# Performance work log

Hardware: AMD Instinct MI355X
Metric: run time of the kernel (lower is better)

The kernel has to match this reference:

```python
import jax, jax.numpy as jnp
import numpy as np
import math

B, T, D, H = 4, 2048, 1024, 16
HD = D // H  # 64

def setup_inputs() -> dict:
    key = jax.random.key(0)
    ks = jax.random.split(key, 11)
    s = 1.0 / math.sqrt(D)
    return {
        "q": jax.random.normal(ks[0], (B, T, D), jnp.float32),
        "k": jax.random.normal(ks[1], (B, T, D), jnp.float32),
        "v": jax.random.normal(ks[2], (B, T, D), jnp.float32),
        "Wq": jax.random.normal(ks[3], (D, D), jnp.float32) * s,
        "bq": jnp.zeros((D,), jnp.float32),
        "Wk": jax.random.normal(ks[4], (D, D), jnp.float32) * s,
        "bk": jnp.zeros((D,), jnp.float32),
        "Wv": jax.random.normal(ks[5], (D, D), jnp.float32) * s,
        "bv": jnp.zeros((D,), jnp.float32),
        "Wo": jax.random.normal(ks[6], (D, D), jnp.float32) * s,
        "bo": jnp.zeros((D,), jnp.float32),
    }

def reference(q, k, v, Wq, bq, Wk, bk, Wv, bv, Wo, bo):
    # Linear projections (torch Linear: x @ W.T + b)
    qp = q @ Wq.T + bq
    kp = k @ Wk.T + bk
    vp = v @ Wv.T + bv
    # [B, T, D] -> [B, H, T, HD]
    def split(x):
        return x.reshape(B, T, H, HD).transpose(0, 2, 1, 3)
    qh, kh, vh = split(qp), split(kp), split(vp)
    # scaled dot-product attention
    score = jnp.einsum('bhqd,bhkd->bhqk', qh, kh) / math.sqrt(HD)
    attn = jax.nn.softmax(score, axis=-1)
    out = jnp.einsum('bhqk,bhkd->bhqd', attn, vh)
    # merge heads and output projection
    out = out.transpose(0, 2, 1, 3).reshape(B, T, D)
    return out @ Wo.T + bo
```

## Files before the change

kernel.cpp:

```cpp
#include <hip/hip_runtime.h>
#include <hip/hip_bf16.h>
#include <stdint.h>

#define B_ 4
#define T_ 2048
#define D_ 1024
#define H_ 16
#define HD_ 64
#define NKT (T_ / 64)

typedef __bf16 bf16;
typedef __bf16 bf16x8 __attribute__((ext_vector_type(8)));
typedef __bf16 bf16x4 __attribute__((ext_vector_type(4)));
typedef float f32x4 __attribute__((ext_vector_type(4)));
typedef uint32_t u32x4 __attribute__((ext_vector_type(4)));

#define QSCALE 0.18033688011112042f

__device__ __forceinline__ float fast_exp2(float x) {
#if __has_builtin(__builtin_amdgcn_exp2f)
    return __builtin_amdgcn_exp2f(x);
#else
    return exp2f(x);
#endif
}

__device__ __forceinline__ void async_load16(const bf16* g, const bf16* lds_uniform) {
    __builtin_amdgcn_global_load_lds(
        (const __attribute__((address_space(1))) uint32_t*)(uintptr_t)g,
        (__attribute__((address_space(3))) uint32_t*)(uintptr_t)lds_uniform,
        16, 0, 0);
}

__device__ __forceinline__ uint32_t pack2_bf16(float lo, float hi) {
    union { uint32_t u; __bf16 h[2]; } r;
    r.h[0] = (__bf16)lo;
    r.h[1] = (__bf16)hi;
    return r.u;
}

__device__ __forceinline__ void permswap16(uint32_t& a, uint32_t& b) {
    asm("v_permlane16_swap_b32 %0, %1" : "+v"(a), "+v"(b));
}

__global__ __launch_bounds__(256) void cast3(const float* __restrict__ s0, bf16* __restrict__ d0,
                                             const float* __restrict__ s1, bf16* __restrict__ d1,
                                             const float* __restrict__ s2, bf16* __restrict__ d2,
                                             int n4) {
    const float* s = blockIdx.y == 0 ? s0 : (blockIdx.y == 1 ? s1 : s2);
    bf16* d = blockIdx.y == 0 ? d0 : (blockIdx.y == 1 ? d1 : d2);
    int i = blockIdx.x * 256 + threadIdx.x;
    if (i < n4) {
        f32x4 v = ((const f32x4*)s)[i];
        bf16x4 o;
        o.x = (bf16)v.x; o.y = (bf16)v.y; o.z = (bf16)v.z; o.w = (bf16)v.w;
        ((bf16x4*)d)[i] = o;
    }
}

__global__ __launch_bounds__(256) void cast4(const float* __restrict__ s0, bf16* __restrict__ d0,
                                             const float* __restrict__ s1, bf16* __restrict__ d1,
                                             const float* __restrict__ s2, bf16* __restrict__ d2,
                                             const float* __restrict__ s3, bf16* __restrict__ d3,
                                             int n4) {
    const float* s = blockIdx.y == 0 ? s0 : (blockIdx.y == 1 ? s1 : (blockIdx.y == 2 ? s2 : s3));
    bf16* d = blockIdx.y == 0 ? d0 : (blockIdx.y == 1 ? d1 : (blockIdx.y == 2 ? d2 : d3));
    int i = blockIdx.x * 256 + threadIdx.x;
    if (i < n4) {
        f32x4 v = ((const f32x4*)s)[i];
        bf16x4 o;
        o.x = (bf16)v.x; o.y = (bf16)v.y; o.z = (bf16)v.z; o.w = (bf16)v.w;
        ((bf16x4*)d)[i] = o;
    }
}

template <typename OutT, int VMODE>
__global__ __launch_bounds__(256) void gemm_nt(const bf16* __restrict__ A,
                                               const bf16* __restrict__ W,
                                               const float* __restrict__ bias,
                                               OutT* __restrict__ C,
                                               int M, int N, int K, float scale) {
    __shared__ bf16 As[2][128 * 32];
    __shared__ bf16 Bs[2][128 * 32];
    const int tid = threadIdx.x;
    const int wid = tid >> 6, lane = tid & 63;
    const int quad = lane >> 4, l15 = lane & 15;
    const int wm = (wid >> 1) * 64, wn = (wid & 1) * 64;
    const int bx = N >> 7;
    const int lin = blockIdx.x;
    const int ty = (lin & 7) + 8 * (lin / (8 * bx));
    const int tx = (lin >> 3) % bx;
    const long rowA0 = (long)ty * 128;
    const long rowB0 = (long)tx * 128;
    const int srow = lane >> 2;
    const int schunk = (lane & 3) * 8;
    const int sbase = (wid * 32) * 32;

    f32x4 acc[4][4];
#pragma unroll
    for (int i = 0; i < 4; i++)
#pragma unroll
        for (int j = 0; j < 4; j++) acc[i][j] = (f32x4){0.f, 0.f, 0.f, 0.f};

#pragma unroll
    for (int s = 0; s < 2; s++) {
        int r = wid * 32 + s * 16 + srow;
        async_load16(&A[(rowA0 + r) * K + schunk], &As[0][sbase + s * 16 * 32]);
        async_load16(&W[(rowB0 + r) * K + schunk], &Bs[0][sbase + s * 16 * 32]);
    }
    __syncthreads();

    const int NIT = K >> 5;
    for (int it = 0; it < NIT; it++) {
        const int cur = it & 1;
        if (it + 1 < NIT) {
            const int k1 = (it + 1) << 5, nb = cur ^ 1;
#pragma unroll
            for (int s = 0; s < 2; s++) {
                int r = wid * 32 + s * 16 + srow;
                async_load16(&A[(rowA0 + r) * K + k1 + schunk], &As[nb][sbase + s * 16 * 32]);
                async_load16(&W[(rowB0 + r) * K + k1 + schunk], &Bs[nb][sbase + s * 16 * 32]);
            }
        }
        bf16x8 af[4], bfr[4];
#pragma unroll
        for (int i = 0; i < 4; i++)
            af[i] = *(const bf16x8*)&As[cur][(wm + i * 16 + l15) * 32 + quad * 8];
#pragma unroll
        for (int j = 0; j < 4; j++)
            bfr[j] = *(const bf16x8*)&Bs[cur][(wn + j * 16 + l15) * 32 + quad * 8];
#pragma unroll
        for (int i = 0; i < 4; i++)
#pragma unroll
            for (int j = 0; j < 4; j++)
                acc[i][j] = __builtin_amdgcn_mfma_f32_16x16x32_bf16(af[i], bfr[j],
                                                                    acc[i][j], 0, 0, 0);
        __syncthreads();
    }

    if constexpr (VMODE == 0) {
#pragma unroll
        for (int i = 0; i < 4; i++) {
            long m = rowA0 + wm + i * 16 + quad * 4;
#pragma unroll
            for (int j = 0; j < 4; j++) {
                long n = rowB0 + wn + j * 16 + l15;
                float bb = bias[n];
#pragma unroll
                for (int r = 0; r < 4; r++) {
                    float v = (acc[i][j][r] + bb) * scale;
                    C[(m + r) * N + n] = (OutT)v;
                }
            }
        }
    } else {
        __shared__ bf16 Tt[128 * 136];
#pragma unroll
        for (int i = 0; i < 4; i++) {
            int ml = wm + i * 16 + quad * 4;
#pragma unroll
            for (int j = 0; j < 4; j++) {
                int nl = wn + j * 16 + l15;
                float bb = bias[rowB0 + nl];
                bf16x4 ov = {(bf16)(acc[i][j][0] + bb), (bf16)(acc[i][j][1] + bb),
                             (bf16)(acc[i][j][2] + bb), (bf16)(acc[i][j][3] + bb)};
                *(bf16x4*)&Tt[nl * 136 + ml] = ov;
            }
        }
        __syncthreads();
        const long bidx = rowA0 >> 11;
        const int t0 = (int)(rowA0 & 2047);
#pragma unroll
        for (int p = 0; p < 8; p++) {
            int nl = p * 16 + (tid >> 4);
            int c = tid & 15;
            bf16x8 val = *(const bf16x8*)&Tt[nl * 136 + c * 8];
            int n = (int)rowB0 + nl;
            long vrow = (bidx * H_ + (n >> 6)) * (long)HD_ + (n & 63);
            int cp = (c & ~3) | ((c & 1) << 1) | ((c & 2) >> 1);
            *(bf16x8*)&((bf16*)C)[vrow * T_ + t0 + cp * 8] = val;
        }
    }
}

__global__ __launch_bounds__(256) void attn_kernel(const bf16* __restrict__ Qp,
                                                   const bf16* __restrict__ Kp,
                                                   const bf16* __restrict__ VT,
                                                   bf16* __restrict__ Op) {
    __shared__ bf16 smem[4][64 * 64];
    const int tid = threadIdx.x;
    const int wid = tid >> 6, lane = tid & 63;
    const int quad = lane >> 4, l15 = lane & 15;
    const int q7 = l15 & 7;
    const int lin = blockIdx.x;
    const int bh = (lin & 7) + 8 * (lin >> 6);
    const int qt = (lin >> 3) & 7;
    const int b = bh >> 4, h = bh & 15;
    const long tok0 = (long)b * T_ + (long)qt * 256 + wid * 64;
    const int hcol = h * HD_;
    const long vrow0 = ((long)bh) * HD_;
    const int g_sw = ((lane & 7) ^ (lane >> 3)) * 8;
    const int srow = lane >> 3;
    const int sbase = (wid * 16) * 64;

    {
        const long krow0 = (long)b * T_;
#pragma unroll
        for (int s = 0; s < 2; s++) {
            int r = wid * 16 + s * 8 + srow;
            async_load16(&Kp[(krow0 + r) * D_ + hcol + g_sw], &smem[0][sbase + s * 8 * 64]);
            async_load16(&VT[(vrow0 + r) * T_ + g_sw], &smem[2][sbase + s * 8 * 64]);
        }
    }

    bf16x8 bq[4][2];
#pragma unroll
    for (int nt = 0; nt < 4; nt++)
#pragma unroll
        for (int ks = 0; ks < 2; ks++)
            bq[nt][ks] = *(const bf16x8*)&Qp[(tok0 + nt * 16 + l15) * D_ + hcol +
                                             ks * 32 + quad * 8];

    f32x4 o[4][4];
#pragma unroll
    for (int mt = 0; mt < 4; mt++)
#pragma unroll
        for (int nt = 0; nt < 4; nt++) o[mt][nt] = (f32x4){0.f, 0.f, 0.f, 0.f};
    float lsum[4] = {0.f, 0.f, 0.f, 0.f};

    __syncthreads();

    for (int kt = 0; kt < NKT; kt++) {
        const int cur = kt & 1;
        if (kt + 1 < NKT) {
            const long krow1 = (long)b * T_ + (long)(kt + 1) * 64;
            const int nb = cur ^ 1;
#pragma unroll
            for (int s = 0; s < 2; s++) {
                int r = wid * 16 + s * 8 + srow;
                async_load16(&Kp[(krow1 + r) * D_ + hcol + g_sw], &smem[nb][sbase + s * 8 * 64]);
                async_load16(&VT[(vrow0 + r) * T_ + (long)(kt + 1) * 64 + g_sw],
                             &smem[2 + nb][sbase + s * 8 * 64]);
            }
        }
        const bf16* Ksc = smem[cur];
        const bf16* Vsc = smem[2 + cur];

        bf16x8 pb0[4];
        {
            uint32_t pA[2][4], pB[2][4];
#pragma unroll
            for (int mt = 0; mt < 2; mt++) {
                bf16x8 ak0 = *(const bf16x8*)&Ksc[(mt * 16 + l15) * 64 + ((quad ^ q7) * 8)];
                bf16x8 ak1 = *(const bf16x8*)&Ksc[(mt * 16 + l15) * 64 + (((4 + quad) ^ q7) * 8)];
#pragma unroll
                for (int nt = 0; nt < 4; nt++) {
                    f32x4 s = {0.f, 0.f, 0.f, 0.f};
                    s = __builtin_amdgcn_mfma_f32_16x16x32_bf16(ak0, bq[nt][0], s, 0, 0, 0);
                    s = __builtin_amdgcn_mfma_f32_16x16x32_bf16(ak1, bq[nt][1], s, 0, 0, 0);
                    float p0 = fast_exp2(s[0]), p1 = fast_exp2(s[1]);
                    float p2 = fast_exp2(s[2]), p3 = fast_exp2(s[3]);
                    lsum[nt] += (p0 + p1) + (p2 + p3);
                    pA[mt][nt] = pack2_bf16(p0, p1);
                    pB[mt][nt] = pack2_bf16(p2, p3);
                }
            }
#pragma unroll
            for (int nt = 0; nt < 4; nt++) {
                permswap16(pA[0][nt], pA[1][nt]);
                permswap16(pB[0][nt], pB[1][nt]);
                u32x4 f = {pA[0][nt], pB[0][nt], pA[1][nt], pB[1][nt]};
                pb0[nt] = __builtin_bit_cast(bf16x8, f);
            }
        }
#pragma unroll
        for (int mt = 0; mt < 4; mt++) {
            bf16x8 av0 = *(const bf16x8*)&Vsc[(mt * 16 + l15) * 64 + ((quad ^ q7) * 8)];
#pragma unroll
            for (int nt = 0; nt < 4; nt++)
                o[mt][nt] = __builtin_amdgcn_mfma_f32_16x16x32_bf16(av0, pb0[nt],
                                                                    o[mt][nt], 0, 0, 0);
        }
        bf16x8 pb1[4];
        {
            uint32_t pA[2][4], pB[2][4];
#pragma unroll
            for (int mt = 0; mt < 2; mt++) {
                bf16x8 ak0 = *(const bf16x8*)&Ksc[((2 + mt) * 16 + l15) * 64 + ((quad ^ q7) * 8)];
                bf16x8 ak1 = *(const bf16x8*)&Ksc[((2 + mt) * 16 + l15) * 64 +
                                                  (((4 + quad) ^ q7) * 8)];
#pragma unroll
                for (int nt = 0; nt < 4; nt++) {
                    f32x4 s = {0.f, 0.f, 0.f, 0.f};
                    s = __builtin_amdgcn_mfma_f32_16x16x32_bf16(ak0, bq[nt][0], s, 0, 0, 0);
                    s = __builtin_amdgcn_mfma_f32_16x16x32_bf16(ak1, bq[nt][1], s, 0, 0, 0);
                    float p0 = fast_exp2(s[0]), p1 = fast_exp2(s[1]);
                    float p2 = fast_exp2(s[2]), p3 = fast_exp2(s[3]);
                    lsum[nt] += (p0 + p1) + (p2 + p3);
                    pA[mt][nt] = pack2_bf16(p0, p1);
                    pB[mt][nt] = pack2_bf16(p2, p3);
                }
            }
#pragma unroll
            for (int nt = 0; nt < 4; nt++) {
                permswap16(pA[0][nt], pA[1][nt]);
                permswap16(pB[0][nt], pB[1][nt]);
                u32x4 f = {pA[0][nt], pB[0][nt], pA[1][nt], pB[1][nt]};
                pb1[nt] = __builtin_bit_cast(bf16x8, f);
            }
        }
#pragma unroll
        for (int mt = 0; mt < 4; mt++) {
            bf16x8 av1 = *(const bf16x8*)&Vsc[(mt * 16 + l15) * 64 + (((4 + quad) ^ q7) * 8)];
#pragma unroll
            for (int nt = 0; nt < 4; nt++)
                o[mt][nt] = __builtin_amdgcn_mfma_f32_16x16x32_bf16(av1, pb1[nt],
                                                                    o[mt][nt], 0, 0, 0);
        }
        __syncthreads();
    }

#pragma unroll
    for (int nt = 0; nt < 4; nt++) {
        lsum[nt] += __shfl_xor(lsum[nt], 16, 64);
        lsum[nt] += __shfl_xor(lsum[nt], 32, 64);
        lsum[nt] = 1.f / lsum[nt];
    }

    bf16* ew = &smem[wid][0];
#pragma unroll
    for (int mt = 0; mt < 4; mt++)
#pragma unroll
        for (int nt = 0; nt < 4; nt++) {
            bf16x4 ov = {(bf16)(o[mt][nt][0] * lsum[nt]), (bf16)(o[mt][nt][1] * lsum[nt]),
                         (bf16)(o[mt][nt][2] * lsum[nt]), (bf16)(o[mt][nt][3] * lsum[nt])};
            *(bf16x4*)&ew[(nt * 16 + l15) * 64 +
                          (((mt * 2 + (quad >> 1)) ^ q7) * 8) + (quad & 1) * 4] = ov;
        }
#pragma unroll
    for (int p2 = 0; p2 < 8; p2++) {
        int q = p2 * 8 + (lane >> 3);
        int dc = lane & 7;
        bf16x8 ov = *(const bf16x8*)&ew[q * 64 + ((dc ^ (q & 7)) * 8)];
        *(bf16x8*)&Op[(tok0 + q) * D_ + hcol + dc * 8] = ov;
    }
}

extern "C" void kernel_launch(void* const* d_in, const int* in_sizes, int n_in,
                              void* d_out, int out_size, void* d_ws, size_t ws_size,
                              hipStream_t stream) {
    const float* q  = (const float*)d_in[0];
    const float* k  = (const float*)d_in[1];
    const float* v  = (const float*)d_in[2];
    const float* Wq = (const float*)d_in[3];
    const float* bq = (const float*)d_in[4];
    const float* Wk = (const float*)d_in[5];
    const float* bk = (const float*)d_in[6];
    const float* Wv = (const float*)d_in[7];
    const float* bv = (const float*)d_in[8];
    const float* Wo = (const float*)d_in[9];
    const float* bo = (const float*)d_in[10];
    float* out = (float*)d_out;

    const size_t MD = (size_t)B_ * T_ * D_;
    const size_t DD = (size_t)D_ * D_;
    char* ws = (char*)d_ws;
    bf16* Xq  = (bf16*)ws; ws += MD * 2;
    bf16* Xk  = (bf16*)ws; ws += MD * 2;
    bf16* Xv  = (bf16*)ws; ws += MD * 2;
    bf16* WqB = (bf16*)ws; ws += DD * 2;
    bf16* WkB = (bf16*)ws; ws += DD * 2;
    bf16* WvB = (bf16*)ws; ws += DD * 2;
    bf16* WoB = (bf16*)ws; ws += DD * 2;
    bf16* Qp  = (bf16*)ws; ws += MD * 2;
    bf16* Kp  = (bf16*)ws; ws += MD * 2;
    bf16* VtG = (bf16*)ws; ws += MD * 2;
    bf16* Op  = (bf16*)ws; ws += MD * 2;

    cast3<<<dim3(MD / 4 / 256, 3), 256, 0, stream>>>(q, Xq, k, Xk, v, Xv, MD / 4);
    cast4<<<dim3(DD / 4 / 256, 4), 256, 0, stream>>>(Wq, WqB, Wk, WkB, Wv, WvB, Wo, WoB, DD / 4);

    const int nblk = (B_ * T_ / 128) * (D_ / 128);
    gemm_nt<bf16, 0><<<nblk, 256, 0, stream>>>(Xq, WqB, bq, Qp, B_ * T_, D_, D_, QSCALE);
    gemm_nt<bf16, 0><<<nblk, 256, 0, stream>>>(Xk, WkB, bk, Kp, B_ * T_, D_, D_, 1.f);
    gemm_nt<bf16, 1><<<nblk, 256, 0, stream>>>(Xv, WvB, bv, VtG, B_ * T_, D_, D_, 1.f);

    attn_kernel<<<B_ * H_ * (T_ / 256), 256, 0, stream>>>(Qp, Kp, VtG, Op);

    gemm_nt<float, 0><<<nblk, 256, 0, stream>>>(Op, WoB, bo, out, B_ * T_, D_, D_, 1.f);
}
```

Measured before the change: 342.8 us.

## Merge QKV GEMMs into one launch and halve attention query tile per block

The three projection GEMMs now run as a single 1536-block launch, with a branch on blockIdx choosing the Q, K or V path. Shared memory is overlaid so the V-transpose staging buffer reuses the A/B tile space. The attention kernel now handles 32 queries per wave (128 per block) instead of 64, which doubles the grid to 1024 blocks, and it adds a launch bound of 4 blocks per CU. The aim is to fill the GPU better and cut launch gaps and tail effects, at the cost of loading each K/V tile twice as often per query.

```diff
diff --git a/kernel.cpp b/kernel.cpp
--- a/kernel.cpp
+++ b/kernel.cpp
@@ -75,19 +75,18 @@
 }
 
 template <typename OutT, int VMODE>
-__global__ __launch_bounds__(256) void gemm_nt(const bf16* __restrict__ A,
-                                               const bf16* __restrict__ W,
-                                               const float* __restrict__ bias,
-                                               OutT* __restrict__ C,
-                                               int M, int N, int K, float scale) {
-    __shared__ bf16 As[2][128 * 32];
-    __shared__ bf16 Bs[2][128 * 32];
+__device__ __forceinline__ void gemm_body(const bf16* __restrict__ A,
+                                          const bf16* __restrict__ W,
+                                          const float* __restrict__ bias,
+                                          OutT* __restrict__ C,
+                                          int lin, float scale,
+                                          bf16* As, bf16* Bs, bf16* Tt) {
+    const int K = D_, N = D_;
     const int tid = threadIdx.x;
     const int wid = tid >> 6, lane = tid & 63;
     const int quad = lane >> 4, l15 = lane & 15;
     const int wm = (wid >> 1) * 64, wn = (wid & 1) * 64;
     const int bx = N >> 7;
-    const int lin = blockIdx.x;
     const int ty = (lin & 7) + 8 * (lin / (8 * bx));
     const int tx = (lin >> 3) % bx;
     const long rowA0 = (long)ty * 128;
@@ -105,30 +104,32 @@
 #pragma unroll
     for (int s = 0; s < 2; s++) {
         int r = wid * 32 + s * 16 + srow;
-        async_load16(&A[(rowA0 + r) * K + schunk], &As[0][sbase + s * 16 * 32]);
-        async_load16(&W[(rowB0 + r) * K + schunk], &Bs[0][sbase + s * 16 * 32]);
+        async_load16(&A[(rowA0 + r) * K + schunk], &As[sbase + s * 16 * 32]);
+        async_load16(&W[(rowB0 + r) * K + schunk], &Bs[sbase + s * 16 * 32]);
     }
     __syncthreads();
 
     const int NIT = K >> 5;
     for (int it = 0; it < NIT; it++) {
         const int cur = it & 1;
+        const int co = cur * (128 * 32);
         if (it + 1 < NIT) {
-            const int k1 = (it + 1) << 5, nb = cur ^ 1;
+            const int k1 = (it + 1) << 5;
+            const int no = (cur ^ 1) * (128 * 32);
 #pragma unroll
             for (int s = 0; s < 2; s++) {
                 int r = wid * 32 + s * 16 + srow;
-                async_load16(&A[(rowA0 + r) * K + k1 + schunk], &As[nb][sbase + s * 16 * 32]);
-                async_load16(&W[(rowB0 + r) * K + k1 + schunk], &Bs[nb][sbase + s * 16 * 32]);
+                async_load16(&A[(rowA0 + r) * K + k1 + schunk], &As[no + sbase + s * 16 * 32]);
+                async_load16(&W[(rowB0 + r) * K + k1 + schunk], &Bs[no + sbase + s * 16 * 32]);
             }
         }
         bf16x8 af[4], bfr[4];
 #pragma unroll
         for (int i = 0; i < 4; i++)
-            af[i] = *(const bf16x8*)&As[cur][(wm + i * 16 + l15) * 32 + quad * 8];
+            af[i] = *(const bf16x8*)&As[co + (wm + i * 16 + l15) * 32 + quad * 8];
 #pragma unroll
         for (int j = 0; j < 4; j++)
-            bfr[j] = *(const bf16x8*)&Bs[cur][(wn + j * 16 + l15) * 32 + quad * 8];
+            bfr[j] = *(const bf16x8*)&Bs[co + (wn + j * 16 + l15) * 32 + quad * 8];
 #pragma unroll
         for (int i = 0; i < 4; i++)
 #pragma unroll
@@ -154,7 +155,6 @@
             }
         }
     } else {
-        __shared__ bf16 Tt[128 * 136];
 #pragma unroll
         for (int i = 0; i < 4; i++) {
             int ml = wm + i * 16 + quad * 4;
@@ -183,20 +183,56 @@
     }
 }
 
-__global__ __launch_bounds__(256) void attn_kernel(const bf16* __restrict__ Qp,
-                                                   const bf16* __restrict__ Kp,
-                                                   const bf16* __restrict__ VT,
-                                                   bf16* __restrict__ Op) {
+__global__ __launch_bounds__(256) void gemm_qkv(const bf16* __restrict__ Xq,
+                                                const bf16* __restrict__ WqB,
+                                                const float* __restrict__ bq,
+                                                bf16* __restrict__ Qp,
+                                                const bf16* __restrict__ Xk,
+                                                const bf16* __restrict__ WkB,
+                                                const float* __restrict__ bk,
+                                                bf16* __restrict__ Kp,
+                                                const bf16* __restrict__ Xv,
+                                                const bf16* __restrict__ WvB,
+                                                const float* __restrict__ bv,
+                                                bf16* __restrict__ VtG) {
+    __shared__ __align__(16) char sm[34816];
+    bf16* As = (bf16*)sm;
+    bf16* Bs = (bf16*)(sm + 16384);
+    bf16* Tt = (bf16*)sm;
+    const int p = blockIdx.x >> 9;
+    const int lin = blockIdx.x & 511;
+    if (p == 0)
+        gemm_body<bf16, 0>(Xq, WqB, bq, Qp, lin, QSCALE, As, Bs, Tt);
+    else if (p == 1)
+        gemm_body<bf16, 0>(Xk, WkB, bk, Kp, lin, 1.f, As, Bs, Tt);
+    else
+        gemm_body<bf16, 1>(Xv, WvB, bv, VtG, lin, 1.f, As, Bs, Tt);
+}
+
+__global__ __launch_bounds__(256) void gemm_out(const bf16* __restrict__ Op,
+                                                const bf16* __restrict__ WoB,
+                                                const float* __restrict__ bo,
+                                                float* __restrict__ out) {
+    __shared__ __align__(16) char sm[32768];
+    bf16* As = (bf16*)sm;
+    bf16* Bs = (bf16*)(sm + 16384);
+    gemm_body<float, 0>(Op, WoB, bo, out, blockIdx.x, 1.f, As, Bs, nullptr);
+}
+
+__global__ __launch_bounds__(256, 4) void attn_kernel(const bf16* __restrict__ Qp,
+                                                      const bf16* __restrict__ Kp,
+                                                      const bf16* __restrict__ VT,
+                                                      bf16* __restrict__ Op) {
     __shared__ bf16 smem[4][64 * 64];
     const int tid = threadIdx.x;
     const int wid = tid >> 6, lane = tid & 63;
     const int quad = lane >> 4, l15 = lane & 15;
     const int q7 = l15 & 7;
     const int lin = blockIdx.x;
-    const int bh = (lin & 7) + 8 * (lin >> 6);
-    const int qt = (lin >> 3) & 7;
+    const int bh = (lin & 7) + 8 * (lin >> 7);
+    const int qt = (lin >> 3) & 15;
     const int b = bh >> 4, h = bh & 15;
-    const long tok0 = (long)b * T_ + (long)qt * 256 + wid * 64;
+    const long tok0 = (long)b * T_ + (long)qt * 128 + wid * 32;
     const int hcol = h * HD_;
     const long vrow0 = ((long)bh) * HD_;
     const int g_sw = ((lane & 7) ^ (lane >> 3)) * 8;
@@ -213,20 +249,20 @@
         }
     }
 
-    bf16x8 bq[4][2];
-#pragma unroll
-    for (int nt = 0; nt < 4; nt++)
+    bf16x8 bq[2][2];
+#pragma unroll
+    for (int nt = 0; nt < 2; nt++)
 #pragma unroll
         for (int ks = 0; ks < 2; ks++)
             bq[nt][ks] = *(const bf16x8*)&Qp[(tok0 + nt * 16 + l15) * D_ + hcol +
                                              ks * 32 + quad * 8];
 
-    f32x4 o[4][4];
+    f32x4 o[4][2];
 #pragma unroll
     for (int mt = 0; mt < 4; mt++)
 #pragma unroll
-        for (int nt = 0; nt < 4; nt++) o[mt][nt] = (f32x4){0.f, 0.f, 0.f, 0.f};
-    float lsum[4] = {0.f, 0.f, 0.f, 0.f};
+        for (int nt = 0; nt < 2; nt++) o[mt][nt] = (f32x4){0.f, 0.f, 0.f, 0.f};
+    float lsum[2] = {0.f, 0.f};
 
     __syncthreads();
 
@@ -246,15 +282,15 @@
         const bf16* Ksc = smem[cur];
         const bf16* Vsc = smem[2 + cur];
 
-        bf16x8 pb0[4];
+        bf16x8 pb0[2];
         {
-            uint32_t pA[2][4], pB[2][4];
+            uint32_t pA[2][2], pB[2][2];
 #pragma unroll
             for (int mt = 0; mt < 2; mt++) {
                 bf16x8 ak0 = *(const bf16x8*)&Ksc[(mt * 16 + l15) * 64 + ((quad ^ q7) * 8)];
                 bf16x8 ak1 = *(const bf16x8*)&Ksc[(mt * 16 + l15) * 64 + (((4 + quad) ^ q7) * 8)];
 #pragma unroll
-                for (int nt = 0; nt < 4; nt++) {
+                for (int nt = 0; nt < 2; nt++) {
                     f32x4 s = {0.f, 0.f, 0.f, 0.f};
                     s = __builtin_amdgcn_mfma_f32_16x16x32_bf16(ak0, bq[nt][0], s, 0, 0, 0);
                     s = __builtin_amdgcn_mfma_f32_16x16x32_bf16(ak1, bq[nt][1], s, 0, 0, 0);
@@ -266,7 +302,7 @@
                 }
             }
 #pragma unroll
-            for (int nt = 0; nt < 4; nt++) {
+            for (int nt = 0; nt < 2; nt++) {
                 permswap16(pA[0][nt], pA[1][nt]);
                 permswap16(pB[0][nt], pB[1][nt]);
                 u32x4 f = {pA[0][nt], pB[0][nt], pA[1][nt], pB[1][nt]};
@@ -277,20 +313,20 @@
         for (int mt = 0; mt < 4; mt++) {
             bf16x8 av0 = *(const bf16x8*)&Vsc[(mt * 16 + l15) * 64 + ((quad ^ q7) * 8)];
 #pragma unroll
-            for (int nt = 0; nt < 4; nt++)
+            for (int nt = 0; nt < 2; nt++)
                 o[mt][nt] = __builtin_amdgcn_mfma_f32_16x16x32_bf16(av0, pb0[nt],
                                                                     o[mt][nt], 0, 0, 0);
         }
-        bf16x8 pb1[4];
+        bf16x8 pb1[2];
         {
-            uint32_t pA[2][4], pB[2][4];
+            uint32_t pA[2][2], pB[2][2];
 #pragma unroll
             for (int mt = 0; mt < 2; mt++) {
                 bf16x8 ak0 = *(const bf16x8*)&Ksc[((2 + mt) * 16 + l15) * 64 + ((quad ^ q7) * 8)];
                 bf16x8 ak1 = *(const bf16x8*)&Ksc[((2 + mt) * 16 + l15) * 64 +
                                                   (((4 + quad) ^ q7) * 8)];
 #pragma unroll
-                for (int nt = 0; nt < 4; nt++) {
+                for (int nt = 0; nt < 2; nt++) {
                     f32x4 s = {0.f, 0.f, 0.f, 0.f};
                     s = __builtin_amdgcn_mfma_f32_16x16x32_bf16(ak0, bq[nt][0], s, 0, 0, 0);
                     s = __builtin_amdgcn_mfma_f32_16x16x32_bf16(ak1, bq[nt][1], s, 0, 0, 0);
@@ -302,7 +338,7 @@
                 }
             }
 #pragma unroll
-            for (int nt = 0; nt < 4; nt++) {
+            for (int nt = 0; nt < 2; nt++) {
                 permswap16(pA[0][nt], pA[1][nt]);
                 permswap16(pB[0][nt], pB[1][nt]);
                 u32x4 f = {pA[0][nt], pB[0][nt], pA[1][nt], pB[1][nt]};
@@ -313,7 +349,7 @@
         for (int mt = 0; mt < 4; mt++) {
             bf16x8 av1 = *(const bf16x8*)&Vsc[(mt * 16 + l15) * 64 + (((4 + quad) ^ q7) * 8)];
 #pragma unroll
-            for (int nt = 0; nt < 4; nt++)
+            for (int nt = 0; nt < 2; nt++)
                 o[mt][nt] = __builtin_amdgcn_mfma_f32_16x16x32_bf16(av1, pb1[nt],
                                                                     o[mt][nt], 0, 0, 0);
         }
@@ -321,7 +357,7 @@
     }
 
 #pragma unroll
-    for (int nt = 0; nt < 4; nt++) {
+    for (int nt = 0; nt < 2; nt++) {
         lsum[nt] += __shfl_xor(lsum[nt], 16, 64);
         lsum[nt] += __shfl_xor(lsum[nt], 32, 64);
         lsum[nt] = 1.f / lsum[nt];
@@ -331,14 +367,14 @@
 #pragma unroll
     for (int mt = 0; mt < 4; mt++)
 #pragma unroll
-        for (int nt = 0; nt < 4; nt++) {
+        for (int nt = 0; nt < 2; nt++) {
             bf16x4 ov = {(bf16)(o[mt][nt][0] * lsum[nt]), (bf16)(o[mt][nt][1] * lsum[nt]),
                          (bf16)(o[mt][nt][2] * lsum[nt]), (bf16)(o[mt][nt][3] * lsum[nt])};
             *(bf16x4*)&ew[(nt * 16 + l15) * 64 +
                           (((mt * 2 + (quad >> 1)) ^ q7) * 8) + (quad & 1) * 4] = ov;
         }
 #pragma unroll
-    for (int p2 = 0; p2 < 8; p2++) {
+    for (int p2 = 0; p2 < 4; p2++) {
         int q = p2 * 8 + (lane >> 3);
         int dc = lane & 7;
         bf16x8 ov = *(const bf16x8*)&ew[q * 64 + ((dc ^ (q & 7)) * 8)];
@@ -380,12 +416,9 @@
     cast3<<<dim3(MD / 4 / 256, 3), 256, 0, stream>>>(q, Xq, k, Xk, v, Xv, MD / 4);
     cast4<<<dim3(DD / 4 / 256, 4), 256, 0, stream>>>(Wq, WqB, Wk, WkB, Wv, WvB, Wo, WoB, DD / 4);
 
-    const int nblk = (B_ * T_ / 128) * (D_ / 128);
-    gemm_nt<bf16, 0><<<nblk, 256, 0, stream>>>(Xq, WqB, bq, Qp, B_ * T_, D_, D_, QSCALE);
-    gemm_nt<bf16, 0><<<nblk, 256, 0, stream>>>(Xk, WkB, bk, Kp, B_ * T_, D_, D_, 1.f);
-    gemm_nt<bf16, 1><<<nblk, 256, 0, stream>>>(Xv, WvB, bv, VtG, B_ * T_, D_, D_, 1.f);
-
-    attn_kernel<<<B_ * H_ * (T_ / 256), 256, 0, stream>>>(Qp, Kp, VtG, Op);
-
-    gemm_nt<float, 0><<<nblk, 256, 0, stream>>>(Op, WoB, bo, out, B_ * T_, D_, D_, 1.f);
-}
+    gemm_qkv<<<3 * 512, 256, 0, stream>>>(Xq, WqB, bq, Qp, Xk, WkB, bk, Kp, Xv, WvB, bv, VtG);
+
+    attn_kernel<<<B_ * H_ * (T_ / 128), 256, 0, stream>>>(Qp, Kp, VtG, Op);
+
+    gemm_out<<<512, 256, 0, stream>>>(Op, WoB, bo, out);
+}
```

Result: faster. 331.8 us (-3.2%).
